# Optimization experiments

Measured on AMD Instinct MI355X. Metric: run time of the kernel, lower is better.

The kernel has to match this reference:

```python
import jax, jax.numpy as jnp
import numpy as np

N, D = 131072, 128   # total nodes, feature size (input_size)
G, L = 512, 448      # num graphs, max padded segment length
EPS = 1e-5


def setup_inputs() -> dict:
    key = jax.random.key(0)
    ks = jax.random.split(key, 8)
    # ragged segment sizes summing exactly to N, each <= L
    rng = np.random.default_rng(0)
    counts = rng.integers(192, 321, size=G)
    diff = N - int(counts.sum())
    idx = rng.integers(0, G, size=abs(diff))
    np.add.at(counts, idx, 1 if diff > 0 else -1)
    assert int(counts.sum()) == N and int(counts.max()) <= L
    batch = jnp.asarray(np.repeat(np.arange(G), counts), dtype=jnp.int32)

    s = 1.0 / np.sqrt(D)
    x = jax.random.normal(ks[0], (N, D), jnp.float32)
    Wk = jax.random.normal(ks[1], (D, D), jnp.float32) * s
    Wq = jax.random.normal(ks[2], (D, D), jnp.float32) * s
    Wv = jax.random.normal(ks[3], (D, D), jnp.float32) * s
    bk = jnp.zeros((D,), jnp.float32)
    bq = jnp.zeros((D,), jnp.float32)
    bv = jnp.zeros((D,), jnp.float32)
    gamma = jnp.ones((D,), jnp.float32)
    beta = jnp.zeros((D,), jnp.float32)
    return {"x": x, "Wk": Wk, "bk": bk, "Wq": Wq, "bq": bq,
            "Wv": Wv, "bv": bv, "gamma": gamma, "beta": beta, "batch": batch}


def reference(x, Wk, bk, Wq, bq, Wv, bv, gamma, beta, batch):
    keys = x @ Wk.T + bk
    query = x @ Wq.T + bq
    values = x @ Wv.T + bv

    counts = jnp.bincount(batch, length=G)                 # [G]
    starts = jnp.cumsum(counts) - counts                   # segment offsets
    pos = jnp.arange(N, dtype=batch.dtype) - starts[batch]  # index within segment

    # scatter ragged nodes into padded [G, L, D] blocks (honors block-diagonal structure)
    kp = jnp.zeros((G, L, D), x.dtype).at[batch, pos].set(keys)
    qp = jnp.zeros((G, L, D), x.dtype).at[batch, pos].set(query)
    vp = jnp.zeros((G, L, D), x.dtype).at[batch, pos].set(values)
    valid = jnp.arange(L)[None, :] < counts[:, None]        # [G, L]

    # NOTE: original computes softmax(K @ Q^T / sqrt(dk)) @ V (keys as rows)
    scale = 1.0 / jnp.sqrt(jnp.asarray(D, x.dtype))
    scores = jnp.einsum('gld,gmd->glm', kp, qp) * scale     # [G, L, L]
    scores = jnp.where(valid[:, None, :], scores, jnp.asarray(-1e9, x.dtype))
    attn = jax.nn.softmax(scores, axis=-1)
    zp = jnp.einsum('glm,gmd->gld', attn, vp)               # [G, L, D]
    z = zp[batch, pos]                                      # back to ragged [N, D]

    h = x + z
    mu = jnp.mean(h, axis=-1, keepdims=True)
    var = jnp.var(h, axis=-1, keepdims=True)
    return (h - mu) / jnp.sqrt(var + EPS) * gamma + beta
```

## Files before the change

kernel.cpp:

```cpp
#include <hip/hip_runtime.h>
#include <hip/hip_bf16.h>

#define N_NODES 131072
#define DIM 128
#define NG 512

typedef __bf16 bf16;
typedef __attribute__((ext_vector_type(8))) __bf16 bf16x8;
typedef __attribute__((ext_vector_type(4))) float f32x4;

#define KSC 0.12753785006196978f

#define WS_STARTS 0
#define WS_WF     8192
#define WS_KB     131072
#define WS_QB     (131072 + 33554432)
#define WS_VTB    (131072 + 2*33554432)

__global__ void seg_starts_kernel(const int* __restrict__ batch, int* __restrict__ starts) {
    int g = threadIdx.x;
    int lo = 0, hi = N_NODES;
    while (lo < hi) { int mid = (lo + hi) >> 1; if (batch[mid] < g) lo = mid + 1; else hi = mid; }
    starts[g] = lo;
    if (g == 0) starts[NG] = N_NODES;
}

__global__ void wconv_kernel(const float* __restrict__ Wk, const float* __restrict__ Wq,
                             const float* __restrict__ Wv, bf16* __restrict__ Wf) {
    int f = blockIdx.x * 256 + threadIdx.x;
    int lane = f & 63, ks = (f >> 6) & 3, n0 = (f >> 8) & 7, mat = f >> 11;
    const float* src = (mat == 0) ? Wk : ((mat == 1) ? Wq : Wv);
    float sc = (mat == 0) ? KSC : 1.0f;
    int col = n0 * 16 + (lane & 15);
    int koff = ks * 32 + (lane >> 4) * 8;
    const float* p = src + col * DIM + koff;
    bf16* dst = Wf + (size_t)f * 8;
    #pragma unroll
    for (int j = 0; j < 8; j++) dst[j] = (bf16)(p[j] * sc);
}

__global__ __launch_bounds__(256) void qkv_kernel(
        const float* __restrict__ x, const bf16* __restrict__ Wf,
        const float* __restrict__ bk, const float* __restrict__ bq, const float* __restrict__ bv,
        bf16* __restrict__ Kb, bf16* __restrict__ Qb, bf16* __restrict__ Vtb) {
    __shared__ bf16 tile[128 * 136];
    const int tid = threadIdx.x;
    const int w = tid >> 6, lane = tid & 63, q = lane >> 4, i = lane & 15;
    const int r0 = blockIdx.x * 128;

    {
        #pragma unroll
        for (int it = 0; it < 16; it++) {
            int e = tid * 4 + it * 1024;
            int row = e >> 7, col = e & 127;
            float4 u = *(const float4*)(x + (size_t)(r0 + row) * DIM + col);
            bf16 b[4] = {(bf16)u.x, (bf16)u.y, (bf16)u.z, (bf16)u.w};
            *(ushort4*)&tile[row * 136 + col] = *(ushort4*)b;
        }
    }
    __syncthreads();

    bf16x8 af[2][4];
    #pragma unroll
    for (int rg = 0; rg < 2; rg++)
        #pragma unroll
        for (int ks = 0; ks < 4; ks++)
            af[rg][ks] = *(const bf16x8*)&tile[(w * 32 + rg * 16 + i) * 136 + ks * 32 + q * 8];
    __syncthreads();

    for (int mat = 0; mat < 3; mat++) {
        const float* bias = (mat == 0) ? bk : ((mat == 1) ? bq : bv);
        const float bscale = (mat == 0) ? KSC : 1.0f;
        for (int n0 = 0; n0 < 8; n0++) {
            int col = n0 * 16 + i;
            float bias_v = bias[col] * bscale;
            f32x4 acc0 = {0,0,0,0}, acc1 = {0,0,0,0};
            #pragma unroll
            for (int ks = 0; ks < 4; ks++) {
                bf16x8 bw = *(const bf16x8*)(Wf + ((size_t)((mat * 8 + n0) * 4 + ks) * 64 + lane) * 8);
                acc0 = __builtin_amdgcn_mfma_f32_16x16x32_bf16(af[0][ks], bw, acc0, 0, 0, 0);
                acc1 = __builtin_amdgcn_mfma_f32_16x16x32_bf16(af[1][ks], bw, acc1, 0, 0, 0);
            }
            #pragma unroll
            for (int rg = 0; rg < 2; rg++) {
                f32x4 a = rg ? acc1 : acc0;
                #pragma unroll
                for (int r = 0; r < 4; r++) {
                    int rowl = w * 32 + rg * 16 + q * 4 + r;
                    bf16 hv = (bf16)(a[r] + bias_v);
                    if (mat < 2) tile[rowl * 136 + col] = hv;
                    else         tile[col * 136 + rowl] = hv;
                }
            }
        }
        __syncthreads();
        {
            int row = tid >> 1, half = tid & 1;
            const uint4* src = (const uint4*)(tile + row * 136 + half * 64);
            uint4* dst;
            if (mat == 0)      dst = (uint4*)(Kb  + (size_t)(r0 + row) * DIM + half * 64);
            else if (mat == 1) dst = (uint4*)(Qb  + (size_t)(r0 + row) * DIM + half * 64);
            else               dst = (uint4*)(Vtb + (size_t)row * N_NODES + r0 + half * 64);
            #pragma unroll
            for (int j = 0; j < 8; j++) dst[j] = src[j];
        }
        __syncthreads();
    }
}

__global__ __launch_bounds__(512, 4) void attn_kernel(
        const float* __restrict__ x,
        const bf16* __restrict__ Kb, const bf16* __restrict__ Qb, const bf16* __restrict__ Vtb,
        const float* __restrict__ gamma, const float* __restrict__ beta,
        const int* __restrict__ starts, float* __restrict__ out) {
    __shared__ bf16 Qs[64 * 136];
    __shared__ bf16 Vts[128 * 72];
    __shared__ bf16 Ps[8 * 16 * 72];

    const int g = blockIdx.y;
    const int seg = starts[g];
    const int c = starts[g + 1] - seg;
    const int l0 = blockIdx.x * 128;
    if (l0 >= c) return;

    const int tid = threadIdx.x;
    const int w = tid >> 6, lane = tid & 63, q = lane >> 4, i = lane & 15;

    bf16x8 afK[4];
    {
        int lrow = l0 + w * 16 + i;
        if (lrow > c - 1) lrow = c - 1;
        const bf16* krow = Kb + (size_t)(seg + lrow) * DIM;
        #pragma unroll
        for (int ks = 0; ks < 4; ks++)
            afK[ks] = *(const bf16x8*)(krow + ks * 32 + q * 8);
    }

    float li[4] = {0.0f, 0.0f, 0.0f, 0.0f};
    f32x4 Oc[8];
    #pragma unroll
    for (int t = 0; t < 8; t++) Oc[t] = (f32x4){0,0,0,0};

    const int mstart = seg & ~7;
    const int nch = (seg - mstart + c + 63) >> 6;
    for (int mc = 0; mc < nch; mc++) {
        const int mbase = mstart + (mc << 6);
        __syncthreads();
        {
            int row = tid >> 3;
            int gr = mbase + row; if (gr > N_NODES - 1) gr = N_NODES - 1;
            const uint4* src = (const uint4*)(Qb + (size_t)gr * DIM);
            #pragma unroll
            for (int p = 0; p < 2; p++) {
                int slot = (tid & 7) + 8 * p;
                *(uint4*)&Qs[row * 136 + slot * 8] = src[slot];
            }
        }
        {
            int d = tid >> 2;
            #pragma unroll
            for (int p = 0; p < 2; p++) {
                int slot = (tid & 3) + 4 * p;
                int mo = mbase + slot * 8; if (mo > N_NODES - 8) mo = N_NODES - 8;
                uint4 v = *(const uint4*)(Vtb + (size_t)d * N_NODES + mo);
                *(uint4*)&Vts[d * 72 + slot * 8] = v;
            }
        }
        __syncthreads();

        f32x4 s[4];
        #pragma unroll
        for (int ti = 0; ti < 4; ti++) {
            f32x4 acc = {0,0,0,0};
            #pragma unroll
            for (int ks = 0; ks < 4; ks++) {
                bf16x8 bq = *(const bf16x8*)&Qs[(ti * 16 + i) * 136 + ks * 32 + q * 8];
                acc = __builtin_amdgcn_mfma_f32_16x16x32_bf16(afK[ks], bq, acc, 0, 0, 0);
            }
            s[ti] = acc;
        }
        if (mc == 0 || mc == nch - 1) {
            #pragma unroll
            for (int ti = 0; ti < 4; ti++) {
                int mg = mbase + ti * 16 + i;
                bool valid = (mg >= seg) && (mg < seg + c);
                #pragma unroll
                for (int r = 0; r < 4; r++)
                    s[ti][r] = valid ? s[ti][r] : -1.0e30f;
            }
        }

        bf16* Pw = Ps + w * (16 * 72);
        #pragma unroll
        for (int ti = 0; ti < 4; ti++)
            #pragma unroll
            for (int r = 0; r < 4; r++) {
                float pv = exp2f(s[ti][r]);
                li[r] += pv;
                Pw[(q * 4 + r) * 72 + ti * 16 + i] = (bf16)pv;
            }

        bf16x8 afP[2];
        #pragma unroll
        for (int k2 = 0; k2 < 2; k2++)
            afP[k2] = *(const bf16x8*)&Pw[i * 72 + k2 * 32 + q * 8];
        #pragma unroll
        for (int dt = 0; dt < 8; dt++) {
            #pragma unroll
            for (int k2 = 0; k2 < 2; k2++) {
                bf16x8 bv = *(const bf16x8*)&Vts[(dt * 16 + i) * 72 + k2 * 32 + q * 8];
                Oc[dt] = __builtin_amdgcn_mfma_f32_16x16x32_bf16(afP[k2], bv, Oc[dt], 0, 0, 0);
            }
        }
    }

    #pragma unroll
    for (int st = 1; st < 16; st <<= 1)
        #pragma unroll
        for (int r = 0; r < 4; r++)
            li[r] += __shfl_xor(li[r], st);

    float gv[8], bvv[8];
    #pragma unroll
    for (int ti = 0; ti < 8; ti++) { gv[ti] = gamma[ti * 16 + i]; bvv[ti] = beta[ti * 16 + i]; }
    for (int r = 0; r < 4; r++) {
        int lg = l0 + w * 16 + q * 4 + r;
        if (lg >= c) continue;
        size_t node = (size_t)(seg + lg);
        float inv = 1.0f / li[r];
        const float* xr = x + node * DIM;
        float h[8], sum = 0.0f, ss = 0.0f;
        #pragma unroll
        for (int ti = 0; ti < 8; ti++) {
            float hv = xr[ti * 16 + i] + Oc[ti][r] * inv;
            h[ti] = hv;
            sum += hv; ss += hv * hv;
        }
        #pragma unroll
        for (int st = 1; st < 16; st <<= 1) {
            sum += __shfl_xor(sum, st);
            ss  += __shfl_xor(ss, st);
        }
        float mu = sum * (1.0f / 128.0f);
        float var = ss * (1.0f / 128.0f) - mu * mu;
        float rstd = rsqrtf(var + 1e-5f);
        float* op = out + node * DIM;
        #pragma unroll
        for (int ti = 0; ti < 8; ti++)
            op[ti * 16 + i] = (h[ti] - mu) * rstd * gv[ti] + bvv[ti];
    }
}

extern "C" void kernel_launch(void* const* d_in, const int* in_sizes, int n_in,
                              void* d_out, int out_size, void* d_ws, size_t ws_size,
                              hipStream_t stream) {
    (void)in_sizes; (void)n_in; (void)out_size; (void)ws_size;
    const float* x     = (const float*)d_in[0];
    const float* Wk    = (const float*)d_in[1];
    const float* bk    = (const float*)d_in[2];
    const float* Wq    = (const float*)d_in[3];
    const float* bq    = (const float*)d_in[4];
    const float* Wv    = (const float*)d_in[5];
    const float* bv    = (const float*)d_in[6];
    const float* gamma = (const float*)d_in[7];
    const float* beta  = (const float*)d_in[8];
    const int*   batch = (const int*)d_in[9];
    float* out = (float*)d_out;

    char* ws = (char*)d_ws;
    int*  starts = (int*)(ws + WS_STARTS);
    bf16* Wf  = (bf16*)(ws + WS_WF);
    bf16* Kb  = (bf16*)(ws + WS_KB);
    bf16* Qb  = (bf16*)(ws + WS_QB);
    bf16* Vtb = (bf16*)(ws + WS_VTB);

    seg_starts_kernel<<<1, 512, 0, stream>>>(batch, starts);
    wconv_kernel<<<24, 256, 0, stream>>>(Wk, Wq, Wv, Wf);
    qkv_kernel<<<1024, 256, 0, stream>>>(x, Wf, bk, bq, bv, Kb, Qb, Vtb);
    attn_kernel<<<dim3(4, NG), 512, 0, stream>>>(x, Kb, Qb, Vtb, gamma, beta, starts, out);
}
```

Measured before the change: 277.9 us.

## Double-buffer attention tiles via async global-to-LDS loads with swizzled layout

Restructures the attention kernel to use 256-thread blocks in which each wave owns 32 key rows, so every Q and V fragment read from LDS is reused across two MFMA row groups. Q and V^T chunks are now double-buffered and filled with global_load_lds direct-to-LDS copies for the next chunk while the current one is computed. The copies go into an XOR-swizzled layout that replaces the padded rows. The goal is to hide global load latency, cut LDS traffic per MFMA, and remove the extra barrier per chunk. The cost is higher register pressure from doubled accumulators, and a reliance on correct waitcnt ordering for the async LDS writes.

New measurement: 277.3 us. About the same (-0.2%).

```diff
diff --git a/kernel.cpp b/kernel.cpp
--- a/kernel.cpp
+++ b/kernel.cpp
@@ -16,6 +16,12 @@
 #define WS_KB     131072
 #define WS_QB     (131072 + 33554432)
 #define WS_VTB    (131072 + 2*33554432)
+
+__device__ __forceinline__ void gl_lds16(const void* g, void* l) {
+    __builtin_amdgcn_global_load_lds(
+        (const __attribute__((address_space(1))) unsigned int*)g,
+        (__attribute__((address_space(3))) unsigned int*)l, 16, 0, 0);
+}
 
 __global__ void seg_starts_kernel(const int* __restrict__ batch, int* __restrict__ starts) {
     int g = threadIdx.x;
@@ -108,14 +114,14 @@
     }
 }
 
-__global__ __launch_bounds__(512, 4) void attn_kernel(
+__global__ __launch_bounds__(256, 2) void attn_kernel(
         const float* __restrict__ x,
         const bf16* __restrict__ Kb, const bf16* __restrict__ Qb, const bf16* __restrict__ Vtb,
         const float* __restrict__ gamma, const float* __restrict__ beta,
         const int* __restrict__ starts, float* __restrict__ out) {
-    __shared__ bf16 Qs[64 * 136];
-    __shared__ bf16 Vts[128 * 72];
-    __shared__ bf16 Ps[8 * 16 * 72];
+    __shared__ bf16 Qs[2][64 * 128];
+    __shared__ bf16 Vts[2][128 * 64];
+    __shared__ bf16 Ps[4][32 * 64];
 
     const int g = blockIdx.y;
     const int seg = starts[g];
@@ -126,90 +132,104 @@
     const int tid = threadIdx.x;
     const int w = tid >> 6, lane = tid & 63, q = lane >> 4, i = lane & 15;
 
-    bf16x8 afK[4];
-    {
-        int lrow = l0 + w * 16 + i;
+    const int mstart = seg & ~7;
+    const int nch = (seg - mstart + c + 63) >> 6;
+
+    auto stage = [&](int buf, int mb) {
+        const int rb = w * 16;
+        #pragma unroll
+        for (int p = 0; p < 4; p++) {
+            int row = rb + p * 4 + (lane >> 4);
+            int gr = mb + row; if (gr > N_NODES - 1) gr = N_NODES - 1;
+            gl_lds16(Qb + (size_t)gr * DIM + (((lane & 15) ^ (row & 7)) << 3),
+                     &Qs[buf][(rb + p * 4) * 128]);
+        }
+        const int db = w * 32;
+        #pragma unroll
+        for (int p = 0; p < 4; p++) {
+            int d = db + p * 8 + (lane >> 3);
+            int mo = mb + (((lane & 7) ^ (d & 7)) << 3);
+            if (mo > N_NODES - 8) mo = N_NODES - 8;
+            gl_lds16(Vtb + (size_t)d * N_NODES + mo,
+                     &Vts[buf][(db + p * 8) * 64]);
+        }
+    };
+
+    stage(0, mstart);
+
+    bf16x8 afK[2][4];
+    #pragma unroll
+    for (int rg = 0; rg < 2; rg++) {
+        int lrow = l0 + w * 32 + rg * 16 + i;
         if (lrow > c - 1) lrow = c - 1;
         const bf16* krow = Kb + (size_t)(seg + lrow) * DIM;
         #pragma unroll
         for (int ks = 0; ks < 4; ks++)
-            afK[ks] = *(const bf16x8*)(krow + ks * 32 + q * 8);
+            afK[rg][ks] = *(const bf16x8*)(krow + ks * 32 + q * 8);
     }
 
-    float li[4] = {0.0f, 0.0f, 0.0f, 0.0f};
-    f32x4 Oc[8];
-    #pragma unroll
-    for (int t = 0; t < 8; t++) Oc[t] = (f32x4){0,0,0,0};
-
-    const int mstart = seg & ~7;
-    const int nch = (seg - mstart + c + 63) >> 6;
+    float li[2][4] = {{0,0,0,0},{0,0,0,0}};
+    f32x4 Oc[2][8];
+    #pragma unroll
+    for (int rg = 0; rg < 2; rg++)
+        #pragma unroll
+        for (int t = 0; t < 8; t++) Oc[rg][t] = (f32x4){0,0,0,0};
+
+    bf16* Pw = Ps[w];
+    const int f7 = i & 7;
+    const int mh = (i >> 3);
+
     for (int mc = 0; mc < nch; mc++) {
+        const int cur = mc & 1;
         const int mbase = mstart + (mc << 6);
         __syncthreads();
-        {
-            int row = tid >> 3;
-            int gr = mbase + row; if (gr > N_NODES - 1) gr = N_NODES - 1;
-            const uint4* src = (const uint4*)(Qb + (size_t)gr * DIM);
-            #pragma unroll
-            for (int p = 0; p < 2; p++) {
-                int slot = (tid & 7) + 8 * p;
-                *(uint4*)&Qs[row * 136 + slot * 8] = src[slot];
-            }
-        }
-        {
-            int d = tid >> 2;
-            #pragma unroll
-            for (int p = 0; p < 2; p++) {
-                int slot = (tid & 3) + 4 * p;
-                int mo = mbase + slot * 8; if (mo > N_NODES - 8) mo = N_NODES - 8;
-                uint4 v = *(const uint4*)(Vtb + (size_t)d * N_NODES + mo);
-                *(uint4*)&Vts[d * 72 + slot * 8] = v;
-            }
-        }
-        __syncthreads();
-
-        f32x4 s[4];
+        if (mc + 1 < nch) stage(cur ^ 1, mbase + 64);
+
+        const bf16* QsB = Qs[cur];
+        const bf16* VtB = Vts[cur];
+
         #pragma unroll
         for (int ti = 0; ti < 4; ti++) {
-            f32x4 acc = {0,0,0,0};
+            f32x4 a0 = {0,0,0,0}, a1 = {0,0,0,0};
             #pragma unroll
             for (int ks = 0; ks < 4; ks++) {
-                bf16x8 bq = *(const bf16x8*)&Qs[(ti * 16 + i) * 136 + ks * 32 + q * 8];
-                acc = __builtin_amdgcn_mfma_f32_16x16x32_bf16(afK[ks], bq, acc, 0, 0, 0);
-            }
-            s[ti] = acc;
-        }
-        if (mc == 0 || mc == nch - 1) {
-            #pragma unroll
-            for (int ti = 0; ti < 4; ti++) {
+                bf16x8 bq = *(const bf16x8*)&QsB[(ti * 16 + i) * 128 + (((ks * 4 + q) ^ f7) << 3)];
+                a0 = __builtin_amdgcn_mfma_f32_16x16x32_bf16(afK[0][ks], bq, a0, 0, 0, 0);
+                a1 = __builtin_amdgcn_mfma_f32_16x16x32_bf16(afK[1][ks], bq, a1, 0, 0, 0);
+            }
+            if (mc == 0 || mc == nch - 1) {
                 int mg = mbase + ti * 16 + i;
-                bool valid = (mg >= seg) && (mg < seg + c);
-                #pragma unroll
-                for (int r = 0; r < 4; r++)
-                    s[ti][r] = valid ? s[ti][r] : -1.0e30f;
-            }
-        }
-
-        bf16* Pw = Ps + w * (16 * 72);
-        #pragma unroll
-        for (int ti = 0; ti < 4; ti++)
+                if (mg < seg || mg >= seg + c) {
+                    a0 = (f32x4){-1.0e30f, -1.0e30f, -1.0e30f, -1.0e30f};
+                    a1 = a0;
+                }
+            }
+            int mhi = 2 * ti + mh;
             #pragma unroll
             for (int r = 0; r < 4; r++) {
-                float pv = exp2f(s[ti][r]);
-                li[r] += pv;
-                Pw[(q * 4 + r) * 72 + ti * 16 + i] = (bf16)pv;
-            }
-
-        bf16x8 afP[2];
-        #pragma unroll
-        for (int k2 = 0; k2 < 2; k2++)
-            afP[k2] = *(const bf16x8*)&Pw[i * 72 + k2 * 32 + q * 8];
+                int lr = q * 4 + r;
+                int sl = ((mhi ^ (lr & 7)) << 3) + f7;
+                float p0 = exp2f(a0[r]); li[0][r] += p0;
+                Pw[lr * 64 + sl] = (bf16)p0;
+                float p1 = exp2f(a1[r]); li[1][r] += p1;
+                Pw[(16 + lr) * 64 + sl] = (bf16)p1;
+            }
+        }
+
+        bf16x8 afP[2][2];
+        #pragma unroll
+        for (int rg = 0; rg < 2; rg++)
+            #pragma unroll
+            for (int k2 = 0; k2 < 2; k2++)
+                afP[rg][k2] = *(const bf16x8*)&Pw[(rg * 16 + i) * 64 + (((k2 * 4 + q) ^ f7) << 3)];
+
         #pragma unroll
         for (int dt = 0; dt < 8; dt++) {
             #pragma unroll
             for (int k2 = 0; k2 < 2; k2++) {
-                bf16x8 bv = *(const bf16x8*)&Vts[(dt * 16 + i) * 72 + k2 * 32 + q * 8];
-                Oc[dt] = __builtin_amdgcn_mfma_f32_16x16x32_bf16(afP[k2], bv, Oc[dt], 0, 0, 0);
+                bf16x8 bv = *(const bf16x8*)&VtB[(dt * 16 + i) * 64 + (((k2 * 4 + q) ^ f7) << 3)];
+                Oc[0][dt] = __builtin_amdgcn_mfma_f32_16x16x32_bf16(afP[0][k2], bv, Oc[0][dt], 0, 0, 0);
+                Oc[1][dt] = __builtin_amdgcn_mfma_f32_16x16x32_bf16(afP[1][k2], bv, Oc[1][dt], 0, 0, 0);
             }
         }
     }
@@ -217,38 +237,42 @@
     #pragma unroll
     for (int st = 1; st < 16; st <<= 1)
         #pragma unroll
-        for (int r = 0; r < 4; r++)
-            li[r] += __shfl_xor(li[r], st);
+        for (int rg = 0; rg < 2; rg++)
+            #pragma unroll
+            for (int r = 0; r < 4; r++)
+                li[rg][r] += __shfl_xor(li[rg][r], st);
 
     float gv[8], bvv[8];
     #pragma unroll
-    for (int ti = 0; ti < 8; ti++) { gv[ti] = gamma[ti * 16 + i]; bvv[ti] = beta[ti * 16 + i]; }
-    for (int r = 0; r < 4; r++) {
-        int lg = l0 + w * 16 + q * 4 + r;
-        if (lg >= c) continue;
-        size_t node = (size_t)(seg + lg);
-        float inv = 1.0f / li[r];
-        const float* xr = x + node * DIM;
-        float h[8], sum = 0.0f, ss = 0.0f;
-        #pragma unroll
-        for (int ti = 0; ti < 8; ti++) {
-            float hv = xr[ti * 16 + i] + Oc[ti][r] * inv;
-            h[ti] = hv;
-            sum += hv; ss += hv * hv;
-        }
-        #pragma unroll
-        for (int st = 1; st < 16; st <<= 1) {
-            sum += __shfl_xor(sum, st);
-            ss  += __shfl_xor(ss, st);
-        }
-        float mu = sum * (1.0f / 128.0f);
-        float var = ss * (1.0f / 128.0f) - mu * mu;
-        float rstd = rsqrtf(var + 1e-5f);
-        float* op = out + node * DIM;
-        #pragma unroll
-        for (int ti = 0; ti < 8; ti++)
-            op[ti * 16 + i] = (h[ti] - mu) * rstd * gv[ti] + bvv[ti];
-    }
+    for (int t = 0; t < 8; t++) { gv[t] = gamma[t * 16 + i]; bvv[t] = beta[t * 16 + i]; }
+    #pragma unroll
+    for (int rg = 0; rg < 2; rg++)
+        for (int r = 0; r < 4; r++) {
+            int lg = l0 + w * 32 + rg * 16 + q * 4 + r;
+            if (lg >= c) continue;
+            size_t node = (size_t)(seg + lg);
+            float inv = 1.0f / li[rg][r];
+            const float* xr = x + node * DIM;
+            float h[8], sum = 0.0f, ss = 0.0f;
+            #pragma unroll
+            for (int t = 0; t < 8; t++) {
+                float hv = xr[t * 16 + i] + Oc[rg][t][r] * inv;
+                h[t] = hv;
+                sum += hv; ss += hv * hv;
+            }
+            #pragma unroll
+            for (int st = 1; st < 16; st <<= 1) {
+                sum += __shfl_xor(sum, st);
+                ss  += __shfl_xor(ss, st);
+            }
+            float mu = sum * (1.0f / 128.0f);
+            float var = ss * (1.0f / 128.0f) - mu * mu;
+            float rstd = rsqrtf(var + 1e-5f);
+            float* op = out + node * DIM;
+            #pragma unroll
+            for (int t = 0; t < 8; t++)
+                op[t * 16 + i] = (h[t] - mu) * rstd * gv[t] + bvv[t];
+        }
 }
 
 extern "C" void kernel_launch(void* const* d_in, const int* in_sizes, int n_in,
@@ -277,5 +301,5 @@
     seg_starts_kernel<<<1, 512, 0, stream>>>(batch, starts);
     wconv_kernel<<<24, 256, 0, stream>>>(Wk, Wq, Wv, Wf);
     qkv_kernel<<<1024, 256, 0, stream>>>(x, Wf, bk, bq, bv, Kb, Qb, Vtb);
-    attn_kernel<<<dim3(4, NG), 512, 0, stream>>>(x, Kb, Qb, Vtb, gamma, beta, starts, out);
-}
+    attn_kernel<<<dim3(4, NG), 256, 0, stream>>>(x, Kb, Qb, Vtb, gamma, beta, starts, out);
+}
```

## Double-buffer Q/V tiles via direct global-to-LDS loads with XOR swizzle

Applied to the files above, without the earlier changes.

Replaces the register-staged Q and V^T tile loads with global_load_lds into double-buffered LDS, prefetching the next chunk while the current one computes. Padded layouts become XOR-swizzled to avoid bank conflicts, and the P scratch now reuses the consumed Q buffer, behind an extra barrier. MFMA phases are wrapped in s_setprio. This hides global load latency and removes one barrier per chunk, at the cost of more LDS (double buffers) and subtle synchronization around reusing the Q buffer for P.

Result: no change. 274.5 us (-1.2%).

```diff
diff --git a/kernel.cpp b/kernel.cpp
--- a/kernel.cpp
+++ b/kernel.cpp
@@ -16,6 +16,12 @@
 #define WS_KB     131072
 #define WS_QB     (131072 + 33554432)
 #define WS_VTB    (131072 + 2*33554432)
+
+__device__ __forceinline__ void gl_lds16(const void* g, void* l) {
+    __builtin_amdgcn_global_load_lds(
+        (const __attribute__((address_space(1))) unsigned int*)g,
+        (__attribute__((address_space(3))) unsigned int*)l, 16, 0, 0);
+}
 
 __global__ void seg_starts_kernel(const int* __restrict__ batch, int* __restrict__ starts) {
     int g = threadIdx.x;
@@ -113,9 +119,8 @@
         const bf16* __restrict__ Kb, const bf16* __restrict__ Qb, const bf16* __restrict__ Vtb,
         const float* __restrict__ gamma, const float* __restrict__ beta,
         const int* __restrict__ starts, float* __restrict__ out) {
-    __shared__ bf16 Qs[64 * 136];
-    __shared__ bf16 Vts[128 * 72];
-    __shared__ bf16 Ps[8 * 16 * 72];
+    __shared__ bf16 Qs[2][64 * 128];
+    __shared__ bf16 Vts[2][128 * 64];
 
     const int g = blockIdx.y;
     const int seg = starts[g];
@@ -126,6 +131,29 @@
     const int tid = threadIdx.x;
     const int w = tid >> 6, lane = tid & 63, q = lane >> 4, i = lane & 15;
 
+    const int mstart = seg & ~7;
+    const int nch = (seg - mstart + c + 63) >> 6;
+
+    auto stage = [&](int buf, int mb) {
+        #pragma unroll
+        for (int p = 0; p < 2; p++) {
+            int row = w * 8 + p * 4 + (lane >> 4);
+            int gr = mb + row; if (gr > N_NODES - 1) gr = N_NODES - 1;
+            gl_lds16(Qb + (size_t)gr * DIM + (((lane & 15) ^ (row & 7)) << 3),
+                     &Qs[buf][(w * 8 + p * 4) * 128]);
+        }
+        #pragma unroll
+        for (int p = 0; p < 2; p++) {
+            int d = w * 16 + p * 8 + (lane >> 3);
+            int mo = mb + (((lane & 7) ^ (d & 7)) << 3);
+            if (mo > N_NODES - 8) mo = N_NODES - 8;
+            gl_lds16(Vtb + (size_t)d * N_NODES + mo,
+                     &Vts[buf][(w * 16 + p * 8) * 64]);
+        }
+    };
+
+    stage(0, mstart);
+
     bf16x8 afK[4];
     {
         int lrow = l0 + w * 16 + i;
@@ -141,77 +169,78 @@
     #pragma unroll
     for (int t = 0; t < 8; t++) Oc[t] = (f32x4){0,0,0,0};
 
-    const int mstart = seg & ~7;
-    const int nch = (seg - mstart + c + 63) >> 6;
+    const int f7 = i & 7;
+    const int mh = (i >> 3);
+
     for (int mc = 0; mc < nch; mc++) {
+        const int cur = mc & 1;
         const int mbase = mstart + (mc << 6);
         __syncthreads();
-        {
-            int row = tid >> 3;
-            int gr = mbase + row; if (gr > N_NODES - 1) gr = N_NODES - 1;
-            const uint4* src = (const uint4*)(Qb + (size_t)gr * DIM);
-            #pragma unroll
-            for (int p = 0; p < 2; p++) {
-                int slot = (tid & 7) + 8 * p;
-                *(uint4*)&Qs[row * 136 + slot * 8] = src[slot];
-            }
-        }
-        {
-            int d = tid >> 2;
-            #pragma unroll
-            for (int p = 0; p < 2; p++) {
-                int slot = (tid & 3) + 4 * p;
-                int mo = mbase + slot * 8; if (mo > N_NODES - 8) mo = N_NODES - 8;
-                uint4 v = *(const uint4*)(Vtb + (size_t)d * N_NODES + mo);
-                *(uint4*)&Vts[d * 72 + slot * 8] = v;
-            }
-        }
-        __syncthreads();
+        if (mc + 1 < nch) stage(cur ^ 1, mbase + 64);
+
+        const bf16* QsB = Qs[cur];
+        const bf16* VtB = Vts[cur];
+        bf16* Pw = &Qs[cur][w * 1024];
 
         f32x4 s[4];
+        __builtin_amdgcn_s_setprio(1);
         #pragma unroll
         for (int ti = 0; ti < 4; ti++) {
             f32x4 acc = {0,0,0,0};
             #pragma unroll
             for (int ks = 0; ks < 4; ks++) {
-                bf16x8 bq = *(const bf16x8*)&Qs[(ti * 16 + i) * 136 + ks * 32 + q * 8];
+                bf16x8 bq = *(const bf16x8*)&QsB[(ti * 16 + i) * 128 + (((ks * 4 + q) ^ f7) << 3)];
                 acc = __builtin_amdgcn_mfma_f32_16x16x32_bf16(afK[ks], bq, acc, 0, 0, 0);
             }
             s[ti] = acc;
         }
+        __builtin_amdgcn_s_setprio(0);
         if (mc == 0 || mc == nch - 1) {
             #pragma unroll
             for (int ti = 0; ti < 4; ti++) {
                 int mg = mbase + ti * 16 + i;
                 bool valid = (mg >= seg) && (mg < seg + c);
-                #pragma unroll
-                for (int r = 0; r < 4; r++)
-                    s[ti][r] = valid ? s[ti][r] : -1.0e30f;
-            }
-        }
-
-        bf16* Pw = Ps + w * (16 * 72);
+                if (!valid) s[ti] = (f32x4){-1.0e30f, -1.0e30f, -1.0e30f, -1.0e30f};
+            }
+        }
         #pragma unroll
         for (int ti = 0; ti < 4; ti++)
             #pragma unroll
             for (int r = 0; r < 4; r++) {
                 float pv = exp2f(s[ti][r]);
                 li[r] += pv;
-                Pw[(q * 4 + r) * 72 + ti * 16 + i] = (bf16)pv;
-            }
+                s[ti][r] = pv;
+            }
+
+        asm volatile("s_waitcnt lgkmcnt(0)" ::: "memory");
+        __builtin_amdgcn_s_barrier();
+        asm volatile("" ::: "memory");
+
+        #pragma unroll
+        for (int ti = 0; ti < 4; ti++) {
+            int mhi = 2 * ti + mh;
+            #pragma unroll
+            for (int r = 0; r < 4; r++) {
+                int lr = q * 4 + r;
+                Pw[lr * 64 + ((mhi ^ (lr & 7)) << 3) + f7] = (bf16)s[ti][r];
+            }
+        }
 
         bf16x8 afP[2];
         #pragma unroll
         for (int k2 = 0; k2 < 2; k2++)
-            afP[k2] = *(const bf16x8*)&Pw[i * 72 + k2 * 32 + q * 8];
+            afP[k2] = *(const bf16x8*)&Pw[i * 64 + (((k2 * 4 + q) ^ f7) << 3)];
+
+        __builtin_amdgcn_s_setprio(1);
         #pragma unroll
         for (int dt = 0; dt < 8; dt++) {
             #pragma unroll
             for (int k2 = 0; k2 < 2; k2++) {
-                bf16x8 bv = *(const bf16x8*)&Vts[(dt * 16 + i) * 72 + k2 * 32 + q * 8];
+                bf16x8 bv = *(const bf16x8*)&VtB[(dt * 16 + i) * 64 + (((k2 * 4 + q) ^ f7) << 3)];
                 Oc[dt] = __builtin_amdgcn_mfma_f32_16x16x32_bf16(afP[k2], bv, Oc[dt], 0, 0, 0);
             }
         }
+        __builtin_amdgcn_s_setprio(0);
     }
 
     #pragma unroll
@@ -222,7 +251,7 @@
 
     float gv[8], bvv[8];
     #pragma unroll
-    for (int ti = 0; ti < 8; ti++) { gv[ti] = gamma[ti * 16 + i]; bvv[ti] = beta[ti * 16 + i]; }
+    for (int t = 0; t < 8; t++) { gv[t] = gamma[t * 16 + i]; bvv[t] = beta[t * 16 + i]; }
     for (int r = 0; r < 4; r++) {
         int lg = l0 + w * 16 + q * 4 + r;
         if (lg >= c) continue;
@@ -231,9 +260,9 @@
         const float* xr = x + node * DIM;
         float h[8], sum = 0.0f, ss = 0.0f;
         #pragma unroll
-        for (int ti = 0; ti < 8; ti++) {
-            float hv = xr[ti * 16 + i] + Oc[ti][r] * inv;
-            h[ti] = hv;
+        for (int t = 0; t < 8; t++) {
+            float hv = xr[t * 16 + i] + Oc[t][r] * inv;
+            h[t] = hv;
             sum += hv; ss += hv * hv;
         }
         #pragma unroll
@@ -246,8 +275,8 @@
         float rstd = rsqrtf(var + 1e-5f);
         float* op = out + node * DIM;
         #pragma unroll
-        for (int ti = 0; ti < 8; ti++)
-            op[ti * 16 + i] = (h[ti] - mu) * rstd * gv[ti] + bvv[ti];
+        for (int t = 0; t < 8; t++)
+            op[t * 16 + i] = (h[t] - mu) * rstd * gv[t] + bvv[t];
     }
 }
 
```
